# Performance work log

Hardware: AMD Instinct MI355X
Metric: run time of the kernel (lower is better)

## Reference

```python
import jax, jax.numpy as jnp
import numpy as np

B, H, W = 64, 250, 250
NUM_PROTOTYPES = 10
FC1_IN = 55815  # 15 * 61 * 61


def _conv(x, w, b, stride, pad):
    y = jax.lax.conv_general_dilated(
        x, w, (stride, stride), [(pad, pad), (pad, pad)],
        dimension_numbers=("NCHW", "OIHW", "NCHW"))
    return y + b[None, :, None, None]


def _maxpool2_s1(x):
    # MaxPool2d(kernel_size=2, stride=1), VALID
    return jax.lax.reduce_window(x, -jnp.inf, jax.lax.max,
                                 (1, 1, 2, 2), (1, 1, 1, 1), "VALID")


def setup_inputs() -> dict:
    key = jax.random.key(0)
    ks = jax.random.split(key, 16)
    f32 = jnp.float32
    def rn(k, shape, fan_in):
        return (jax.random.normal(k, shape, dtype=f32) / np.sqrt(fan_in)).astype(f32)
    return {
        "x": jax.random.normal(ks[0], (B, 3, H, W), dtype=f32),
        "conv1_w": rn(ks[1], (6, 3, 5, 5), 3 * 25),
        "conv1_b": jnp.zeros((6,), f32),
        "conv2_w": rn(ks[2], (15, 6, 3, 3), 6 * 9),
        "conv2_b": jnp.zeros((15,), f32),
        "fc1_w": rn(ks[3], (120, FC1_IN), FC1_IN),
        "fc1_b": jnp.zeros((120,), f32),
        "fc2_w": rn(ks[4], (84, 120), 120),
        "fc2_b": jnp.zeros((84,), f32),
        "fc3_w": rn(ks[5], (1, 84), 84),
        "fc3_b": jnp.zeros((1,), f32),
        "prototypes": jax.random.normal(ks[6], (NUM_PROTOTYPES, 1), dtype=f32),
        "kh_w": rn(ks[7], (1, NUM_PROTOTYPES), NUM_PROTOTYPES),
        "kh_b": jnp.zeros((1,), f32),
    }


def reference(x, conv1_w, conv1_b, conv2_w, conv2_b,
              fc1_w, fc1_b, fc2_w, fc2_b, fc3_w, fc3_b,
              prototypes, kh_w, kh_b):
    # Dropout layers are identity at inference.
    h = jax.nn.relu(_conv(x, conv1_w, conv1_b, stride=2, pad=1))  # [B,6,124,124]
    h = _maxpool2_s1(h)                                           # [B,6,123,123]
    h = jax.nn.relu(_conv(h, conv2_w, conv2_b, stride=2, pad=1))  # [B,15,62,62]
    h = _maxpool2_s1(h)                                           # [B,15,61,61]
    h = h.reshape(h.shape[0], -1)                                 # [B,55815]
    h = jax.nn.relu(h @ fc1_w.T + fc1_b)
    h = jax.nn.relu(h @ fc2_w.T + fc2_b)
    z = h @ fc3_w.T + fc3_b                                       # [B,1]
    # Quantum kernel closed form: 4 wires each apply RY(z) then RY(-p);
    # |<0000|psi>| = prod_i cos((z - p)/2) = cos((z - p)/2)^4.
    kernel_sim = jnp.cos((z - prototypes[:, 0][None, :]) * 0.5) ** 4  # [B,P]
    logits = kernel_sim @ kh_w.T + kh_b                           # [B,1]
    probs = jax.nn.sigmoid(logits)
    return jnp.concatenate([probs, 1.0 - probs], axis=-1)         # [B,2]
```

## Files before the change

### kernel.cpp

```cpp
#include <hip/hip_runtime.h>
#include <hip/hip_bf16.h>
#include <math.h>


#define KTOT 55815
#define KTOT_PAD 55872
#define P1H 123
#define P2H 61
#define KC 64
#define KSPAN 256
#define NCHUNK 219

__global__ __launch_bounds__(256) void conv1_pool(
    const float* __restrict__ x, const float* __restrict__ w,
    const float* __restrict__ bias, float* __restrict__ out) {
  __shared__ float smem[6 * 32 * 65];
  const int b = blockIdx.y;
  const int ytile = blockIdx.x >> 1, xtile = blockIdx.x & 1;
  const int cy_base = 31 * ytile;
  const int cx_base = xtile ? 62 : 0;
  const int tid = threadIdx.x;
  const int q = tid >> 4;
  const int st = tid & 15;
  const int gy0 = 2 * cy_base - 1;
  const int s0 = 2 * cx_base - 4;
  const float* xb = x + b * 187500;
  const int cyA = cy_base + 2 * q;
  const bool vA = (cyA < 124), vB = (cyA + 1 < 124);

  float accA[6][4], accB[6][4];
#pragma unroll
  for (int oc = 0; oc < 6; ++oc) {
    const float bv = bias[oc];
#pragma unroll
    for (int p = 0; p < 4; ++p) { accA[oc][p] = bv; accB[oc][p] = bv; }
  }

  float4 rr[9];
  {
    const float* xc = xb;
#pragma unroll
    for (int s = 0; s < 9; ++s) {
      const int idx = tid + 256 * s;
      float4 v = {0.f, 0.f, 0.f, 0.f};
      if (idx < 67 * 34) {
        const int row = idx / 34, j = idx - row * 34;
        const int gy = gy0 + row, gx = s0 + 4 * j;
        if (gy >= 0 && gy < 250) {
          const float* rp = xc + gy * 250;
          if (gx >= 0 && gx + 3 < 250) {
            v = *reinterpret_cast<const float4*>(rp + gx);
          } else if (gx + 3 >= 0 && gx < 250) {
            v.x = (gx + 0 >= 0 && gx + 0 < 250) ? rp[gx + 0] : 0.f;
            v.y = (gx + 1 >= 0 && gx + 1 < 250) ? rp[gx + 1] : 0.f;
            v.z = (gx + 2 >= 0 && gx + 2 < 250) ? rp[gx + 2] : 0.f;
            v.w = (gx + 3 >= 0 && gx + 3 < 250) ? rp[gx + 3] : 0.f;
          }
        }
      }
      rr[s] = v;
    }
  }

  for (int ic = 0; ic < 3; ++ic) {
    __syncthreads();
#pragma unroll
    for (int s = 0; s < 9; ++s) {
      const int idx = tid + 256 * s;
      if (idx < 67 * 34) {
        const int row = idx / 34, j = idx - row * 34;
        const int gj = j ^ ((j >> 3) & 1);
        *reinterpret_cast<float4*>(&smem[row * 136 + 4 * gj]) = rr[s];
      }
    }
    __syncthreads();
    if (ic < 2) {
      const float* xc = xb + (ic + 1) * 62500;
#pragma unroll
      for (int s = 0; s < 9; ++s) {
        const int idx = tid + 256 * s;
        float4 v = {0.f, 0.f, 0.f, 0.f};
        if (idx < 67 * 34) {
          const int row = idx / 34, j = idx - row * 34;
          const int gy = gy0 + row, gx = s0 + 4 * j;
          if (gy >= 0 && gy < 250) {
            const float* rp = xc + gy * 250;
            if (gx >= 0 && gx + 3 < 250) {
              v = *reinterpret_cast<const float4*>(rp + gx);
            } else if (gx + 3 >= 0 && gx < 250) {
              v.x = (gx + 0 >= 0 && gx + 0 < 250) ? rp[gx + 0] : 0.f;
              v.y = (gx + 1 >= 0 && gx + 1 < 250) ? rp[gx + 1] : 0.f;
              v.z = (gx + 2 >= 0 && gx + 2 < 250) ? rp[gx + 2] : 0.f;
              v.w = (gx + 3 >= 0 && gx + 3 < 250) ? rp[gx + 3] : 0.f;
            }
          }
        }
        rr[s] = v;
      }
    }
#pragma unroll
    for (int ii = 0; ii < 7; ++ii) {
      const int row = 4 * q + ii;
      float r16[16];
#pragma unroll
      for (int qq = 0; qq < 4; ++qq) {
        const int c = 2 * st + qq;
        const int gc = c ^ ((c >> 3) & 1);
        const float4 v =
            *reinterpret_cast<const float4*>(&smem[row * 136 + 4 * gc]);
        r16[4 * qq + 0] = v.x; r16[4 * qq + 1] = v.y;
        r16[4 * qq + 2] = v.z; r16[4 * qq + 3] = v.w;
      }
      if (ii <= 4) {
#pragma unroll
        for (int oc = 0; oc < 6; ++oc) {
          const float* wp = w + oc * 75 + ic * 25 + ii * 5;
#pragma unroll
          for (int kx = 0; kx < 5; ++kx) {
            const float wv = wp[kx];
#pragma unroll
            for (int p = 0; p < 4; ++p)
              accA[oc][p] = fmaf(r16[2 * p + 3 + kx], wv, accA[oc][p]);
          }
        }
      }
      if (ii >= 2) {
#pragma unroll
        for (int oc = 0; oc < 6; ++oc) {
          const float* wp = w + oc * 75 + ic * 25 + (ii - 2) * 5;
#pragma unroll
          for (int kx = 0; kx < 5; ++kx) {
            const float wv = wp[kx];
#pragma unroll
            for (int p = 0; p < 4; ++p)
              accB[oc][p] = fmaf(r16[2 * p + 3 + kx], wv, accB[oc][p]);
          }
        }
      }
    }
  }

  __syncthreads();
#pragma unroll
  for (int oc = 0; oc < 6; ++oc)
#pragma unroll
    for (int p = 0; p < 4; ++p) {
      smem[(oc * 32 + 2 * q + 0) * 65 + 4 * st + p] =
          vA ? fmaxf(accA[oc][p], 0.f) : 0.f;
      smem[(oc * 32 + 2 * q + 1) * 65 + 4 * st + p] =
          vB ? fmaxf(accB[oc][p], 0.f) : 0.f;
    }
  __syncthreads();

  for (int idx = tid; idx < 31 * 63; idx += 256) {
    const int pyl = idx / 63, pxl = idx % 63;
    const int py = cy_base + pyl;
    const int px = cx_base + pxl;
    if (py > 122) continue;
    if (xtile == 1 && (pxl == 0 || px > 122)) continue;
    float* ob = out + ((size_t)(b * P1H + py) * P1H + px) * 6;
    float v[6];
#pragma unroll
    for (int oc = 0; oc < 6; ++oc) {
      const float* c0 = &smem[(oc * 32 + pyl) * 65];
      const float* c1 = &smem[(oc * 32 + pyl + 1) * 65];
      v[oc] = fmaxf(fmaxf(c0[pxl], c0[pxl + 1]), fmaxf(c1[pxl], c1[pxl + 1]));
    }
    float2 o0 = {v[0], v[1]}, o1 = {v[2], v[3]}, o2 = {v[4], v[5]};
    *reinterpret_cast<float2*>(ob + 0) = o0;
    *reinterpret_cast<float2*>(ob + 2) = o1;
    *reinterpret_cast<float2*>(ob + 4) = o2;
  }
}

__global__ __launch_bounds__(256, 2) void conv2_pool(
    const float* __restrict__ in, const float* __restrict__ w,
    const float* __restrict__ bias, float* __restrict__ A) {
  __shared__ float cs[15][16][16];
  const int b = blockIdx.y;
  const int ty = blockIdx.x / 5, tx = blockIdx.x % 5;
  const int py0 = ty * 15, px0 = tx * 15;
  const int tid = threadIdx.x;
  const int cyl = tid >> 4, cxl = tid & 15;
  const int cy = py0 + cyl, cx = px0 + cxl;
  const float* ib = in + (size_t)b * (P1H * P1H * 6);
  const bool cv = (cy < 62) && (cx < 62);
  const int iy0 = 2 * cy - 1, ix0 = 2 * cx - 1;

  float rin[54];
#pragma unroll
  for (int ky = 0; ky < 3; ++ky) {
    const int iy = iy0 + ky;
#pragma unroll
    for (int kx = 0; kx < 3; ++kx) {
      const int ix = ix0 + kx;
      const int e = (ky * 3 + kx) * 6;
      const bool ok = cv && (iy >= 0) && (iy < P1H) && (ix >= 0) && (ix < P1H);
      if (ok) {
        const float* p = ib + ((size_t)iy * P1H + ix) * 6;
        const float2 v0 = *reinterpret_cast<const float2*>(p + 0);
        const float2 v1 = *reinterpret_cast<const float2*>(p + 2);
        const float2 v2 = *reinterpret_cast<const float2*>(p + 4);
        rin[e + 0] = v0.x; rin[e + 1] = v0.y; rin[e + 2] = v1.x;
        rin[e + 3] = v1.y; rin[e + 4] = v2.x; rin[e + 5] = v2.y;
      } else {
        rin[e + 0] = 0.f; rin[e + 1] = 0.f; rin[e + 2] = 0.f;
        rin[e + 3] = 0.f; rin[e + 4] = 0.f; rin[e + 5] = 0.f;
      }
    }
  }
#pragma unroll
  for (int oc = 0; oc < 15; ++oc) {
    float a = bias[oc];
#pragma unroll
    for (int ic = 0; ic < 6; ++ic)
#pragma unroll
      for (int ky = 0; ky < 3; ++ky)
#pragma unroll
        for (int kx = 0; kx < 3; ++kx)
          a = fmaf(rin[(ky * 3 + kx) * 6 + ic],
                   w[oc * 54 + ic * 9 + ky * 3 + kx], a);
    cs[oc][cyl][cxl] = fmaxf(a, 0.f);
  }
  __syncthreads();
  if (tid < 225) {
    const int pyl = tid / 15, pxl = tid % 15;
    const int py = py0 + pyl, px = px0 + pxl;
    if (py < P2H && px < P2H) {
      float* ob = A + (size_t)b * KTOT_PAD;
#pragma unroll
      for (int oc = 0; oc < 15; ++oc) {
        const float v = fmaxf(fmaxf(cs[oc][pyl][pxl], cs[oc][pyl][pxl + 1]),
                              fmaxf(cs[oc][pyl + 1][pxl], cs[oc][pyl + 1][pxl + 1]));
        ob[oc * (P2H * P2H) + py * P2H + px] = v;
      }
    }
  }
}

__global__ __launch_bounds__(256) void fc1_partial(
    const float* __restrict__ A, const float* __restrict__ W,
    float* __restrict__ part) {
  __shared__ float As[64 * KC];
  __shared__ float Ws[120 * KC];
  const int tid = threadIdx.x;
  const int chunk = blockIdx.x;
  const int lane = tid & 63;
  const int wave = __builtin_amdgcn_readfirstlane(tid >> 6);
  const int mg = lane >> 3, ng = lane & 7;
  const int n0 = wave * 32;

  float acc[8][4];
#pragma unroll
  for (int r = 0; r < 8; ++r)
#pragma unroll
    for (int s = 0; s < 4; ++s) acc[r][s] = 0.0f;

  for (int half = 0; half < 4; ++half) {
    const int k0 = chunk * KSPAN + half * KC;
    const bool full = (k0 + KC <= KTOT);
    __syncthreads();

    for (int idx = tid; idx < 64 * 16; idx += 256) {
      const int m = idx >> 4, j = idx & 15;
      const int kg = k0 + 4 * j;
      float4 v;
      if (full || kg + 3 < KTOT) {
        v = *reinterpret_cast<const float4*>(A + (size_t)m * KTOT_PAD + kg);
      } else {
        v.x = (kg + 0 < KTOT) ? A[(size_t)m * KTOT_PAD + kg + 0] : 0.f;
        v.y = (kg + 1 < KTOT) ? A[(size_t)m * KTOT_PAD + kg + 1] : 0.f;
        v.z = (kg + 2 < KTOT) ? A[(size_t)m * KTOT_PAD + kg + 2] : 0.f;
        v.w = (kg + 3 < KTOT) ? A[(size_t)m * KTOT_PAD + kg + 3] : 0.f;
      }
      const int slot = (j & 8) | ((j & 7) ^ ((m >> 3) & 7));
      *reinterpret_cast<float4*>(&As[m * KC + 4 * slot]) = v;
    }
    if (full) {
      for (int idx = tid; idx < 120 * KC; idx += 256) {
        const int n = idx >> 6, k = idx & 63;
        const int j = k >> 2, q = k & 3;
        const int slot = (j & 8) | ((j & 7) ^ ((n >> 2) & 7));
        Ws[n * KC + 4 * slot + q] = W[(size_t)n * KTOT + k0 + k];
      }
    } else {
      for (int idx = tid; idx < 120 * KC; idx += 256) {
        const int n = idx >> 6, k = idx & 63;
        const int j = k >> 2, q = k & 3;
        const int slot = (j & 8) | ((j & 7) ^ ((n >> 2) & 7));
        const int kg = k0 + k;
        Ws[n * KC + 4 * slot + q] = (kg < KTOT) ? W[(size_t)n * KTOT + kg] : 0.f;
      }
    }
    __syncthreads();

    const float* Abase = As + mg * 8 * KC;
    const float* Wbase = Ws + (n0 + ng * 4) * KC;
#pragma unroll
    for (int k4 = 0; k4 < KC / 4; ++k4) {
      const int sA = 4 * ((k4 & 8) | ((k4 & 7) ^ mg));
      const int sW = 4 * ((k4 & 8) | ((k4 & 7) ^ ng));
      float4 a[8], wv[4];
#pragma unroll
      for (int r = 0; r < 8; ++r)
        a[r] = *reinterpret_cast<const float4*>(Abase + r * KC + sA);
#pragma unroll
      for (int s = 0; s < 4; ++s)
        wv[s] = *reinterpret_cast<const float4*>(Wbase + s * KC + sW);
#pragma unroll
      for (int r = 0; r < 8; ++r)
#pragma unroll
        for (int s = 0; s < 4; ++s) {
          float t = acc[r][s];
          t = fmaf(a[r].x, wv[s].x, t);
          t = fmaf(a[r].y, wv[s].y, t);
          t = fmaf(a[r].z, wv[s].z, t);
          t = fmaf(a[r].w, wv[s].w, t);
          acc[r][s] = t;
        }
    }
  }

  if (n0 + 4 * ng <= 116) {
    float* pb = part + (size_t)chunk * 7680 + n0 + 4 * ng;
#pragma unroll
    for (int r = 0; r < 8; ++r) {
      const float4 v = {acc[r][0], acc[r][1], acc[r][2], acc[r][3]};
      *reinterpret_cast<float4*>(pb + (mg * 8 + r) * 120) = v;
    }
  }
}

__global__ __launch_bounds__(256) void fc1_reduce(
    const float* __restrict__ part, const float* __restrict__ bias,
    float* __restrict__ h1) {
  __shared__ float red[8][32];
  const int tid = threadIdx.x;
  const int q = tid >> 5, l = tid & 31;
  const int t = blockIdx.x * 32 + l;
  float s = 0.0f;
  for (int c = q; c < NCHUNK; c += 8) s += part[(size_t)c * 7680 + t];
  red[q][l] = s;
  __syncthreads();
  if (q == 0) {
    float v = red[0][l] + red[1][l] + red[2][l] + red[3][l] +
              red[4][l] + red[5][l] + red[6][l] + red[7][l] + bias[t % 120];
    h1[t] = fmaxf(v, 0.0f);
  }
}

__global__ __launch_bounds__(256) void fc2_kernel(
    const float* __restrict__ h1, const float* __restrict__ W,
    const float* __restrict__ bias, float* __restrict__ h2) {
  __shared__ float hs[64][121];
  const int tid = threadIdx.x;
  for (int i = tid; i < 7680; i += 256) hs[i / 120][i % 120] = h1[i];
  __syncthreads();
  const int m = tid & 63;
  const int j = blockIdx.x * 4 + __builtin_amdgcn_readfirstlane(tid >> 6);
  const float* wj = W + j * 120;
  float a = bias[j];
  for (int k = 0; k < 120; ++k) a = fmaf(hs[m][k], wj[k], a);
  h2[m * 84 + j] = fmaxf(a, 0.0f);
}

__global__ void final_kernel(
    const float* __restrict__ h2, const float* __restrict__ w3,
    const float* __restrict__ b3, const float* __restrict__ proto,
    const float* __restrict__ khw, const float* __restrict__ khb,
    float* __restrict__ out) {
  const int m = threadIdx.x;
  const float* h = h2 + m * 84;
  float z = b3[0];
  for (int k = 0; k < 84; ++k) z = fmaf(h[k], w3[k], z);
  float logit = khb[0];
#pragma unroll
  for (int p = 0; p < 10; ++p) {
    const float c = cosf((z - proto[p]) * 0.5f);
    const float c2 = c * c;
    logit = fmaf(c2 * c2, khw[p], logit);
  }
  const float pr = 1.0f / (1.0f + expf(-logit));
  out[m * 2 + 0] = pr;
  out[m * 2 + 1] = 1.0f - pr;
}

extern "C" void kernel_launch(void* const* d_in, const int* in_sizes, int n_in,
                              void* d_out, int out_size, void* d_ws, size_t ws_size,
                              hipStream_t stream) {
  const float* x    = (const float*)d_in[0];
  const float* w1   = (const float*)d_in[1];
  const float* b1   = (const float*)d_in[2];
  const float* w2   = (const float*)d_in[3];
  const float* b2   = (const float*)d_in[4];
  const float* fw1  = (const float*)d_in[5];
  const float* fb1  = (const float*)d_in[6];
  const float* fw2  = (const float*)d_in[7];
  const float* fb2  = (const float*)d_in[8];
  const float* fw3  = (const float*)d_in[9];
  const float* fb3  = (const float*)d_in[10];
  const float* prot = (const float*)d_in[11];
  const float* khw  = (const float*)d_in[12];
  const float* khb  = (const float*)d_in[13];
  float* out = (float*)d_out;

  float* ws = (float*)d_ws;
  float* pool1 = ws;
  float* part  = ws;
  float* A     = ws + 5809536;
  float* h1    = A + 3575808;
  float* h2    = h1 + 7680;

  conv1_pool <<<dim3(8, 64), 256, 0, stream>>>(x, w1, b1, pool1);
  conv2_pool <<<dim3(25, 64), 256, 0, stream>>>(pool1, w2, b2, A);
  fc1_partial<<<dim3(NCHUNK), 256, 0, stream>>>(A, fw1, part);
  fc1_reduce <<<dim3(240), 256, 0, stream>>>(part, fb1, h1);
  fc2_kernel <<<dim3(21), 256, 0, stream>>>(h1, fw2, fb2, h2);
  final_kernel<<<dim3(1), 64, 0, stream>>>(h2, fw3, fb3, prot, khw, khb, out);
}
```

Measured before the change: 109.9 us.

## Double-buffer fc1 tiles and stage them with direct global-to-LDS loads

The fc1 partial-GEMM kernel now keeps two LDS buffers and issues the next K-slice's loads before computing the current one, so memory latency overlaps with FMA work. Full tiles are loaded with global_load_lds (direct global-to-LDS), with pre-swizzled source addresses that reproduce the XOR layout; the tail tile still uses the guarded register path. This doubles LDS use per block, which may reduce occupancy. W rows are loaded 4 bytes per lane, so many small transactions are issued.

```diff
diff --git a/kernel.cpp b/kernel.cpp
--- a/kernel.cpp
+++ b/kernel.cpp
@@ -241,8 +241,8 @@
 __global__ __launch_bounds__(256) void fc1_partial(
     const float* __restrict__ A, const float* __restrict__ W,
     float* __restrict__ part) {
-  __shared__ float As[64 * KC];
-  __shared__ float Ws[120 * KC];
+  __shared__ float As[2][64 * KC];
+  __shared__ float Ws[2][120 * KC];
   const int tid = threadIdx.x;
   const int chunk = blockIdx.x;
   const int lane = tid & 63;
@@ -250,22 +250,38 @@
   const int mg = lane >> 3, ng = lane & 7;
   const int n0 = wave * 32;
 
-  float acc[8][4];
-#pragma unroll
-  for (int r = 0; r < 8; ++r)
-#pragma unroll
-    for (int s = 0; s < 4; ++s) acc[r][s] = 0.0f;
-
-  for (int half = 0; half < 4; ++half) {
-    const int k0 = chunk * KSPAN + half * KC;
-    const bool full = (k0 + KC <= KTOT);
-    __syncthreads();
-
+  auto stage_async = [&](int buf, int k0) {
+#pragma unroll
+    for (int s = 0; s < 4; ++s) {
+      const int q4 = (s * 4 + wave) * 64 + lane;
+      const int m = q4 >> 4, j = q4 & 15;
+      const int jinv = (j & 8) | ((j & 7) ^ ((m >> 3) & 7));
+      const float* src = A + (size_t)m * KTOT_PAD + k0 + 4 * jinv;
+      __builtin_amdgcn_global_load_lds(
+          (const __attribute__((address_space(1))) void*)src,
+          (__attribute__((address_space(3))) void*)&As[buf][(s * 4 + wave) * 256],
+          16, 0, 0);
+    }
+#pragma unroll
+    for (int s = 0; s < 30; ++s) {
+      const int n = wave + 4 * s;
+      const int key = (n >> 2) & 7;
+      const int j = lane >> 2, qq = lane & 3;
+      const int kinv = 4 * ((j & 8) | ((j & 7) ^ key)) + qq;
+      const float* src = W + (size_t)n * KTOT + k0 + kinv;
+      __builtin_amdgcn_global_load_lds(
+          (const __attribute__((address_space(1))) void*)src,
+          (__attribute__((address_space(3))) void*)&Ws[buf][n * KC],
+          4, 0, 0);
+    }
+  };
+
+  auto stage_guarded = [&](int buf, int k0) {
     for (int idx = tid; idx < 64 * 16; idx += 256) {
       const int m = idx >> 4, j = idx & 15;
       const int kg = k0 + 4 * j;
       float4 v;
-      if (full || kg + 3 < KTOT) {
+      if (kg + 3 < KTOT) {
         v = *reinterpret_cast<const float4*>(A + (size_t)m * KTOT_PAD + kg);
       } else {
         v.x = (kg + 0 < KTOT) ? A[(size_t)m * KTOT_PAD + kg + 0] : 0.f;
@@ -274,28 +290,27 @@
         v.w = (kg + 3 < KTOT) ? A[(size_t)m * KTOT_PAD + kg + 3] : 0.f;
       }
       const int slot = (j & 8) | ((j & 7) ^ ((m >> 3) & 7));
-      *reinterpret_cast<float4*>(&As[m * KC + 4 * slot]) = v;
-    }
-    if (full) {
-      for (int idx = tid; idx < 120 * KC; idx += 256) {
-        const int n = idx >> 6, k = idx & 63;
-        const int j = k >> 2, q = k & 3;
-        const int slot = (j & 8) | ((j & 7) ^ ((n >> 2) & 7));
-        Ws[n * KC + 4 * slot + q] = W[(size_t)n * KTOT + k0 + k];
-      }
-    } else {
-      for (int idx = tid; idx < 120 * KC; idx += 256) {
-        const int n = idx >> 6, k = idx & 63;
-        const int j = k >> 2, q = k & 3;
-        const int slot = (j & 8) | ((j & 7) ^ ((n >> 2) & 7));
-        const int kg = k0 + k;
-        Ws[n * KC + 4 * slot + q] = (kg < KTOT) ? W[(size_t)n * KTOT + kg] : 0.f;
-      }
-    }
-    __syncthreads();
-
-    const float* Abase = As + mg * 8 * KC;
-    const float* Wbase = Ws + (n0 + ng * 4) * KC;
+      *reinterpret_cast<float4*>(&As[buf][m * KC + 4 * slot]) = v;
+    }
+    for (int idx = tid; idx < 120 * KC; idx += 256) {
+      const int n = idx >> 6, k = idx & 63;
+      const int j = k >> 2, qq = k & 3;
+      const int slot = (j & 8) | ((j & 7) ^ ((n >> 2) & 7));
+      const int kg = k0 + k;
+      Ws[buf][n * KC + 4 * slot + qq] =
+          (kg < KTOT) ? W[(size_t)n * KTOT + kg] : 0.f;
+    }
+  };
+
+  float acc[8][4];
+#pragma unroll
+  for (int r = 0; r < 8; ++r)
+#pragma unroll
+    for (int s = 0; s < 4; ++s) acc[r][s] = 0.0f;
+
+  auto computeBuf = [&](int buf) {
+    const float* Abase = &As[buf][mg * 8 * KC];
+    const float* Wbase = &Ws[buf][(n0 + ng * 4) * KC];
 #pragma unroll
     for (int k4 = 0; k4 < KC / 4; ++k4) {
       const int sA = 4 * ((k4 & 8) | ((k4 & 7) ^ mg));
@@ -319,6 +334,24 @@
           acc[r][s] = t;
         }
     }
+  };
+
+  const int kbase = chunk * KSPAN;
+  {
+    const int k0 = kbase;
+    if (k0 + KC <= KTOT) stage_async(0, k0); else stage_guarded(0, k0);
+  }
+  __syncthreads();
+
+  for (int h = 0; h < 4; ++h) {
+    const int buf = h & 1;
+    if (h < 3) {
+      const int k1 = kbase + (h + 1) * KC;
+      if (k1 + KC <= KTOT) stage_async(buf ^ 1, k1);
+      else stage_guarded(buf ^ 1, k1);
+    }
+    computeBuf(buf);
+    __syncthreads();
   }
 
   if (n0 + 4 * ng <= 116) {
```

Result: slower. 112.1 us (+2.0%).
